# Kernel optimization log

Measured on AMD Instinct MI355X. Metric: run time of the kernel, lower is better.

The kernel has to match this reference:

```python
import jax, jax.numpy as jnp
import numpy as np

N_GAUSS = 1024
IMG = 192
TANFOV = 0.5  # tan(FoV/2), both axes
ZNEAR, ZFAR = 0.01, 100.0

C0 = 0.28209479177387814
C1 = 0.4886025119029199
C2 = (1.0925484305920792, -1.0925484305920792, 0.31539156525252005, -1.0925484305920792, 0.5462742152960396)
C3 = (-0.5900435899266435, 2.890611442640554, -0.4570457994644658, 0.3731763325901154, -0.4570457994644658, 1.445305721320277, -0.5900435899266435)


def _eval_sh3(sh, d):
    # sh: [N,16,3] coeffs, d: [N,3] unit dirs -> clamped rgb [N,3]
    x, y, z = d[:, 0:1], d[:, 1:2], d[:, 2:3]
    xx, yy, zz = x * x, y * y, z * z
    xy, yz, xz = x * y, y * z, x * z
    res = (C0 * sh[:, 0]
           - C1 * y * sh[:, 1] + C1 * z * sh[:, 2] - C1 * x * sh[:, 3]
           + C2[0] * xy * sh[:, 4] + C2[1] * yz * sh[:, 5]
           + C2[2] * (2.0 * zz - xx - yy) * sh[:, 6]
           + C2[3] * xz * sh[:, 7] + C2[4] * (xx - yy) * sh[:, 8]
           + C3[0] * y * (3.0 * xx - yy) * sh[:, 9]
           + C3[1] * xy * z * sh[:, 10]
           + C3[2] * y * (4.0 * zz - xx - yy) * sh[:, 11]
           + C3[3] * z * (2.0 * zz - 3.0 * xx - 3.0 * yy) * sh[:, 12]
           + C3[4] * x * (4.0 * zz - xx - yy) * sh[:, 13]
           + C3[5] * z * (xx - yy) * sh[:, 14]
           + C3[6] * x * (xx - yy - 3.0 * zz) * sh[:, 15])
    return jnp.maximum(res + 0.5, 0.0)


def _quat_to_rot(q):
    r, x, y, z = q[:, 0], q[:, 1], q[:, 2], q[:, 3]
    return jnp.stack([
        1 - 2 * (y * y + z * z), 2 * (x * y - r * z), 2 * (x * z + r * y),
        2 * (x * y + r * z), 1 - 2 * (x * x + z * z), 2 * (y * z - r * x),
        2 * (x * z - r * y), 2 * (y * z + r * x), 1 - 2 * (x * x + y * y),
    ], axis=-1).reshape(-1, 3, 3)


def setup_inputs() -> dict:
    key = jax.random.key(0)
    ks = jax.random.split(key, 6)
    xy = jax.random.uniform(ks[0], (N_GAUSS, 2), minval=-2.0, maxval=2.0)
    z = jax.random.uniform(ks[1], (N_GAUSS, 1), minval=2.0, maxval=10.0)
    means3D = jnp.concatenate([xy, z], axis=1)
    scales = jax.random.uniform(ks[2], (N_GAUSS, 3), minval=0.01, maxval=0.08)
    q = jax.random.normal(ks[3], (N_GAUSS, 4))
    rotations = q / jnp.linalg.norm(q, axis=1, keepdims=True)
    opacities = jax.random.uniform(ks[4], (N_GAUSS, 1), minval=0.1, maxval=0.99)
    shs = jax.random.normal(ks[5], (N_GAUSS, 16, 3)) * 0.3
    viewmatrix = jnp.eye(4, dtype=jnp.float32)
    proj = np.zeros((4, 4), np.float32)
    proj[0, 0] = 1.0 / TANFOV
    proj[1, 1] = 1.0 / TANFOV
    proj[2, 2] = ZFAR / (ZFAR - ZNEAR)
    proj[2, 3] = -ZFAR * ZNEAR / (ZFAR - ZNEAR)
    proj[3, 2] = 1.0
    return dict(means3D=means3D, scales=scales, rotations=rotations,
                opacities=opacities, shs=shs, viewmatrix=viewmatrix,
                projmatrix=jnp.asarray(proj), campos=jnp.zeros(3, jnp.float32),
                bg_color=jnp.zeros(3, jnp.float32),
                image_height=IMG, image_width=IMG)


def reference(means3D, scales, rotations, opacities, shs, viewmatrix,
              projmatrix, campos, bg_color, image_height, image_width):
    H, W = int(image_height), int(image_width)
    fx = W / (2.0 * TANFOV)
    fy = H / (2.0 * TANFOV)
    N = means3D.shape[0]

    # SH -> RGB (convert_SHs_python branch, active_sh_degree = 3)
    dir_pp = means3D - campos[None, :]
    dir_pp = dir_pp / jnp.linalg.norm(dir_pp, axis=1, keepdims=True)
    colors = _eval_sh3(shs, dir_pp)  # [N,3]

    # 3D covariance Sigma = (R S)(R S)^T  (scale_modifier = 1.0)
    R = _quat_to_rot(rotations)
    M = R * scales[:, None, :]
    cov3d = jnp.einsum('nij,nkj->nik', M, M)  # [N,3,3]

    # projection of means
    hom = jnp.concatenate([means3D, jnp.ones((N, 1), means3D.dtype)], axis=1)
    p_view = hom @ viewmatrix.T
    depth = p_view[:, 2]
    p_hom = hom @ projmatrix.T
    p_proj = p_hom[:, :3] / (p_hom[:, 3:4] + 1e-7)
    gx = ((p_proj[:, 0] + 1.0) * W - 1.0) * 0.5  # ndc2Pix
    gy = ((p_proj[:, 1] + 1.0) * H - 1.0) * 0.5
    means2D = jnp.stack([gx, gy], axis=1)

    in_front = depth > 0.2
    tz = jnp.where(in_front, depth, 1.0)
    lim = 1.3 * TANFOV
    tx = jnp.clip(p_view[:, 0] / tz, -lim, lim) * tz
    ty = jnp.clip(p_view[:, 1] / tz, -lim, lim) * tz

    # EWA splatting: J (top 2 rows) composed with view rotation
    zeros = jnp.zeros_like(tz)
    J = jnp.stack([
        jnp.stack([fx / tz, zeros, -fx * tx / (tz * tz)], axis=-1),
        jnp.stack([zeros, fy / tz, -fy * ty / (tz * tz)], axis=-1),
    ], axis=1)  # [N,2,3]
    T = jnp.einsum('nij,jk->nik', J, viewmatrix[:3, :3])
    cov2d = jnp.einsum('nij,njk,nlk->nil', T, cov3d, T)  # [N,2,2]
    a = cov2d[:, 0, 0] + 0.3  # low-pass filter on diagonal
    b = cov2d[:, 0, 1]
    c = cov2d[:, 1, 1] + 0.3

    det = a * c - b * b
    pos_det = det > 0
    inv_det = jnp.where(pos_det, 1.0 / jnp.where(pos_det, det, 1.0), 0.0)
    conA, conB, conC = c * inv_det, -b * inv_det, a * inv_det

    mid = 0.5 * (a + c)
    lam = mid + jnp.sqrt(jnp.maximum(mid * mid - det, 0.1))
    visible = in_front & pos_det
    radii = jnp.where(visible, jnp.ceil(3.0 * jnp.sqrt(lam)), 0.0)
    visibility_filter = radii > 0

    # per-pixel depth-sorted alpha compositing (dense stand-in for tiles)
    yy, xx = jnp.meshgrid(jnp.arange(H, dtype=means3D.dtype),
                          jnp.arange(W, dtype=means3D.dtype), indexing='ij')
    px = xx.reshape(-1)
    py = yy.reshape(-1)
    dx = gx[None, :] - px[:, None]  # [P,N]
    dy = gy[None, :] - py[:, None]
    power = (-0.5 * (conA[None, :] * dx * dx + conC[None, :] * dy * dy)
             - conB[None, :] * dx * dy)
    keep = ((jnp.abs(dx) <= radii[None, :]) & (jnp.abs(dy) <= radii[None, :])
            & visible[None, :] & (power <= 0.0))
    alpha = jnp.minimum(0.99, opacities[:, 0][None, :] * jnp.exp(jnp.minimum(power, 0.0)))
    alpha = jnp.where(keep & (alpha >= 1.0 / 255.0), alpha, 0.0)

    order = jnp.argsort(jnp.where(visible, depth, jnp.inf))
    a_s = alpha[:, order]
    Tcum = jnp.cumprod(1.0 - a_s, axis=1)
    T_before = jnp.concatenate(
        [jnp.ones((a_s.shape[0], 1), a_s.dtype), Tcum[:, :-1]], axis=1)
    wgt = a_s * T_before
    img = wgt @ colors[order] + Tcum[:, -1:] * bg_color[None, :]
    rendered = img.reshape(H, W, 3).transpose(2, 0, 1)  # CHW like torch
    return rendered, radii.astype(jnp.int32), visibility_filter, means2D
```

## Files before the change

kernel.cpp:

```cpp
#include <hip/hip_runtime.h>

#define NG      1024
#define W_IMG   192
#define H_IMG   192
#define HW      (W_IMG * H_IMG)
#define TILES_X 24
#define TILES_Y 24
#define NTILES  (TILES_X * TILES_Y)
#define TPB     256
#define TPBK    4
#define NBLK    (NTILES / TPBK)

__global__ __launch_bounds__(TPB, 1) void render_fused(
    const float* __restrict__ means3D, const float* __restrict__ scales,
    const float* __restrict__ rotations, const float* __restrict__ opacities,
    const float* __restrict__ shs, const float* __restrict__ viewm,
    const float* __restrict__ projm, const float* __restrict__ campos,
    const float* __restrict__ bg, float* __restrict__ outp)
{
    __shared__ float4 sg0[NG];
    __shared__ float4 sg1[NG];
    __shared__ float4 sg2[NG];
    __shared__ unsigned long long skey[TPBK][NG];
    __shared__ unsigned short     ssrt[TPBK][NG];

    const int t = threadIdx.x;

    const float V0 = viewm[0],  V1 = viewm[1],  V2  = viewm[2],  V3  = viewm[3];
    const float V4 = viewm[4],  V5 = viewm[5],  V6  = viewm[6],  V7  = viewm[7];
    const float V8 = viewm[8],  V9 = viewm[9],  V10 = viewm[10], V11 = viewm[11];
    const float P0 = projm[0],  P1 = projm[1],  P2  = projm[2],  P3  = projm[3];
    const float P4 = projm[4],  P5 = projm[5],  P6  = projm[6],  P7  = projm[7];
    const float P12 = projm[12], P13 = projm[13], P14 = projm[14], P15 = projm[15];
    const float CX = campos[0], CY = campos[1], CZ = campos[2];

#pragma unroll
    for (int j = 0; j < NG / TPB; ++j) {
        const int i = t + j * TPB;

        const float mx = means3D[i * 3 + 0];
        const float my = means3D[i * 3 + 1];
        const float mz = means3D[i * 3 + 2];

        float dxc = mx - CX, dyc = my - CY, dzc = mz - CZ;
        float nrm = sqrtf(dxc * dxc + dyc * dyc + dzc * dzc);
        float x = dxc / nrm, y = dyc / nrm, z = dzc / nrm;
        float xx = x * x, yy = y * y, zz = z * z;
        float xy = x * y, yz = y * z, xz = x * z;

        float basis[16];
        basis[0]  = 0.28209479177387814f;
        basis[1]  = -0.4886025119029199f * y;
        basis[2]  =  0.4886025119029199f * z;
        basis[3]  = -0.4886025119029199f * x;
        basis[4]  =  1.0925484305920792f * xy;
        basis[5]  = -1.0925484305920792f * yz;
        basis[6]  =  0.31539156525252005f * (2.f * zz - xx - yy);
        basis[7]  = -1.0925484305920792f * xz;
        basis[8]  =  0.5462742152960396f * (xx - yy);
        basis[9]  = -0.5900435899266435f * y * (3.f * xx - yy);
        basis[10] =  2.890611442640554f  * xy * z;
        basis[11] = -0.4570457994644658f * y * (4.f * zz - xx - yy);
        basis[12] =  0.3731763325901154f * z * (2.f * zz - 3.f * xx - 3.f * yy);
        basis[13] = -0.4570457994644658f * x * (4.f * zz - xx - yy);
        basis[14] =  1.445305721320277f  * z * (xx - yy);
        basis[15] = -0.5900435899266435f * x * (xx - yy - 3.f * zz);

        float sh[48];
        const float4* shv = (const float4*)shs + i * 12;
#pragma unroll
        for (int w = 0; w < 12; ++w) {
            float4 q4 = shv[w];
            sh[4 * w + 0] = q4.x; sh[4 * w + 1] = q4.y;
            sh[4 * w + 2] = q4.z; sh[4 * w + 3] = q4.w;
        }
        float cr = 0.f, cg = 0.f, cb = 0.f;
#pragma unroll
        for (int k = 0; k < 16; ++k) {
            float b = basis[k];
            cr += b * sh[3 * k + 0];
            cg += b * sh[3 * k + 1];
            cb += b * sh[3 * k + 2];
        }
        cr = fmaxf(cr + 0.5f, 0.f);
        cg = fmaxf(cg + 0.5f, 0.f);
        cb = fmaxf(cb + 0.5f, 0.f);

        const float4 q = ((const float4*)rotations)[i];
        float qr = q.x, qx = q.y, qy = q.z, qz = q.w;
        float sx = scales[i * 3 + 0], sy = scales[i * 3 + 1], sz = scales[i * 3 + 2];
        float R00 = 1.f - 2.f * (qy * qy + qz * qz), R01 = 2.f * (qx * qy - qr * qz), R02 = 2.f * (qx * qz + qr * qy);
        float R10 = 2.f * (qx * qy + qr * qz), R11 = 1.f - 2.f * (qx * qx + qz * qz), R12 = 2.f * (qy * qz - qr * qx);
        float R20 = 2.f * (qx * qz - qr * qy), R21 = 2.f * (qy * qz + qr * qx), R22 = 1.f - 2.f * (qx * qx + qy * qy);
        float M00 = R00 * sx, M01 = R01 * sy, M02 = R02 * sz;
        float M10 = R10 * sx, M11 = R11 * sy, M12 = R12 * sz;
        float M20 = R20 * sx, M21 = R21 * sy, M22 = R22 * sz;
        float S00 = M00 * M00 + M01 * M01 + M02 * M02;
        float S01 = M00 * M10 + M01 * M11 + M02 * M12;
        float S02 = M00 * M20 + M01 * M21 + M02 * M22;
        float S11 = M10 * M10 + M11 * M11 + M12 * M12;
        float S12 = M10 * M20 + M11 * M21 + M12 * M22;
        float S22 = M20 * M20 + M21 * M21 + M22 * M22;

        float pv0 = V0 * mx + V1 * my + V2  * mz + V3;
        float pv1 = V4 * mx + V5 * my + V6  * mz + V7;
        float pv2 = V8 * mx + V9 * my + V10 * mz + V11;
        float ph0 = P0  * mx + P1  * my + P2  * mz + P3;
        float ph1 = P4  * mx + P5  * my + P6  * mz + P7;
        float ph3 = P12 * mx + P13 * my + P14 * mz + P15;
        float pp0 = ph0 / (ph3 + 1e-7f);
        float pp1 = ph1 / (ph3 + 1e-7f);
        float gx = ((pp0 + 1.f) * (float)W_IMG - 1.f) * 0.5f;
        float gy = ((pp1 + 1.f) * (float)H_IMG - 1.f) * 0.5f;

        float depth = pv2;
        bool in_front = depth > 0.2f;
        float tz = in_front ? depth : 1.f;
        const float lim = 1.3f * 0.5f;
        float txv = fminf(fmaxf(pv0 / tz, -lim), lim) * tz;
        float tyv = fminf(fmaxf(pv1 / tz, -lim), lim) * tz;
        const float fx = (float)W_IMG / (2.f * 0.5f);
        const float fy = (float)H_IMG / (2.f * 0.5f);
        float J00 = fx / tz, J02 = -fx * txv / (tz * tz);
        float J11 = fy / tz, J12 = -fy * tyv / (tz * tz);

        float T00 = J00 * V0 + J02 * V8;
        float T01 = J00 * V1 + J02 * V9;
        float T02 = J00 * V2 + J02 * V10;
        float T10 = J11 * V4 + J12 * V8;
        float T11 = J11 * V5 + J12 * V9;
        float T12 = J11 * V6 + J12 * V10;

        float u0 = T00 * S00 + T01 * S01 + T02 * S02;
        float u1 = T00 * S01 + T01 * S11 + T02 * S12;
        float u2 = T00 * S02 + T01 * S12 + T02 * S22;
        float w0 = T10 * S00 + T11 * S01 + T12 * S02;
        float w1 = T10 * S01 + T11 * S11 + T12 * S12;
        float w2 = T10 * S02 + T11 * S12 + T12 * S22;
        float c00 = u0 * T00 + u1 * T01 + u2 * T02;
        float c01 = u0 * T10 + u1 * T11 + u2 * T12;
        float c11 = w0 * T10 + w1 * T11 + w2 * T12;

        float a = c00 + 0.3f;
        float b = c01;
        float c = c11 + 0.3f;
        float det = a * c - b * b;
        bool pos_det = det > 0.f;
        float inv_det = pos_det ? 1.f / det : 0.f;
        float conA = c * inv_det, conB = -b * inv_det, conC = a * inv_det;
        float mid = 0.5f * (a + c);
        float lam = mid + sqrtf(fmaxf(mid * mid - det, 0.1f));
        bool visible = in_front && pos_det;
        float radii = visible ? ceilf(3.f * sqrtf(lam)) : 0.f;

        float opa = opacities[i];

        sg0[i] = make_float4(gx, gy, radii, visible ? opa : 0.f);
        sg1[i] = make_float4(conA, conB, conC, depth);
        sg2[i] = make_float4(cr, cg, cb, 0.f);

        if (blockIdx.x == 0) {
            outp[3 * HW + i]              = radii;
            outp[3 * HW + NG + i]         = (radii > 0.f) ? 1.f : 0.f;
            outp[3 * HW + 2 * NG + 2 * i]     = gx;
            outp[3 * HW + 2 * NG + 2 * i + 1] = gy;
        }
    }
    __syncthreads();

    const int wave = t >> 6;
    const int lane = t & 63;
    const int tile = blockIdx.x * TPBK + wave;
    const int tileX = tile % TILES_X;
    const int tileY = tile / TILES_X;
    const float tx0 = (float)(tileX * 8);
    const float ty0 = (float)(tileY * 8);

    int m = 0;
#pragma unroll 4
    for (int it = 0; it < NG / 64; ++it) {
        const int g = it * 64 + lane;
        float4 g0 = sg0[g];
        bool hit = (g0.w > 0.f) &&
                   (g0.x >= tx0 - g0.z) && (g0.x <= tx0 + 7.f + g0.z) &&
                   (g0.y >= ty0 - g0.z) && (g0.y <= ty0 + 7.f + g0.z);
        unsigned long long mask = __ballot(hit);
        if (hit) {
            int pos = m + __popcll(mask & ((1ULL << lane) - 1ULL));
            skey[wave][pos] =
                ((unsigned long long)__float_as_uint(sg1[g].w) << 32) | (unsigned)g;
        }
        m += __popcll(mask);
    }
    __syncthreads();

    for (int s = lane; s < m; s += 64) {
        const unsigned long long ks = skey[wave][s];
        int rank = 0;
        for (int j2 = 0; j2 < m; ++j2)
            rank += (skey[wave][j2] < ks) ? 1 : 0;
        ssrt[wave][rank] = (unsigned short)(ks & 0xFFFFu);
    }
    __syncthreads();

    const int lx = lane & 7, ly = lane >> 3;
    const int pxi = tileX * 8 + lx;
    const int pyi = tileY * 8 + ly;
    const float px = (float)pxi, py = (float)pyi;

    float T = 1.f, accR = 0.f, accG = 0.f, accB = 0.f;
    for (int k = 0; k < m; ++k) {
        const int gi = ssrt[wave][k];
        float4 g0 = sg0[gi];
        float4 g1 = sg1[gi];
        float4 g2 = sg2[gi];
        float dx = g0.x - px, dy = g0.y - py;
        bool cover = (fabsf(dx) <= g0.z) && (fabsf(dy) <= g0.z);
        float power = -0.5f * (g1.x * dx * dx + g1.z * dy * dy) - g1.y * dx * dy;
        float alpha = fminf(0.99f, g0.w * __expf(fminf(power, 0.f)));
        bool keep = cover && (power <= 0.f) && (alpha >= (1.f / 255.f));
        alpha = keep ? alpha : 0.f;
        float w = alpha * T;
        accR += w * g2.x;
        accG += w * g2.y;
        accB += w * g2.z;
        T *= (1.f - alpha);
    }

    const int pix = pyi * W_IMG + pxi;
    outp[pix]          = accR + T * bg[0];
    outp[HW + pix]     = accG + T * bg[1];
    outp[2 * HW + pix] = accB + T * bg[2];
}

extern "C" void kernel_launch(void* const* d_in, const int* in_sizes, int n_in,
                              void* d_out, int out_size, void* d_ws, size_t ws_size,
                              hipStream_t stream)
{
    const float* means3D   = (const float*)d_in[0];
    const float* scales    = (const float*)d_in[1];
    const float* rotations = (const float*)d_in[2];
    const float* opacities = (const float*)d_in[3];
    const float* shs       = (const float*)d_in[4];
    const float* viewm     = (const float*)d_in[5];
    const float* projm     = (const float*)d_in[6];
    const float* campos    = (const float*)d_in[7];
    const float* bg        = (const float*)d_in[8];

    float* outp = (float*)d_out;

    render_fused<<<NBLK, TPB, 0, stream>>>(
        means3D, scales, rotations, opacities, shs, viewm, projm, campos,
        bg, outp);
}
```

Baseline: 88.67 us.

## Evaluate SH colors only for per-tile hit Gaussians after sorting

Moves the spherical-harmonic color evaluation out of the per-block preprocessing of all 1024 Gaussians. Colors are now computed only for the Gaussians that hit each wave's tile, after sorting, and cached in shared memory up to a cap, with a fallback that recomputes them inline beyond the cap. The sort key is also narrowed from 64-bit to a 32-bit depth plus a separate index array, with explicit index tie-breaking. The aim is to cut redundant SH work and the 48-float global load per Gaussian that every block repeated; the cost is divergent per-tile evaluation and possible inline recomputation in the compositing loop for crowded tiles.

```diff
diff --git a/kernel.cpp b/kernel.cpp
--- a/kernel.cpp
+++ b/kernel.cpp
@@ -10,6 +10,59 @@
 #define TPB     256
 #define TPBK    4
 #define NBLK    (NTILES / TPBK)
+#define CMAX    256
+
+__device__ __forceinline__ float3 eval_sh3(
+    const float* __restrict__ shs, const float* __restrict__ means3D,
+    float CX, float CY, float CZ, int i)
+{
+    const float mx = means3D[i * 3 + 0];
+    const float my = means3D[i * 3 + 1];
+    const float mz = means3D[i * 3 + 2];
+    float dxc = mx - CX, dyc = my - CY, dzc = mz - CZ;
+    float nrm = sqrtf(dxc * dxc + dyc * dyc + dzc * dzc);
+    float x = dxc / nrm, y = dyc / nrm, z = dzc / nrm;
+    float xx = x * x, yy = y * y, zz = z * z;
+    float xy = x * y, yz = y * z, xz = x * z;
+
+    float basis[16];
+    basis[0]  = 0.28209479177387814f;
+    basis[1]  = -0.4886025119029199f * y;
+    basis[2]  =  0.4886025119029199f * z;
+    basis[3]  = -0.4886025119029199f * x;
+    basis[4]  =  1.0925484305920792f * xy;
+    basis[5]  = -1.0925484305920792f * yz;
+    basis[6]  =  0.31539156525252005f * (2.f * zz - xx - yy);
+    basis[7]  = -1.0925484305920792f * xz;
+    basis[8]  =  0.5462742152960396f * (xx - yy);
+    basis[9]  = -0.5900435899266435f * y * (3.f * xx - yy);
+    basis[10] =  2.890611442640554f  * xy * z;
+    basis[11] = -0.4570457994644658f * y * (4.f * zz - xx - yy);
+    basis[12] =  0.3731763325901154f * z * (2.f * zz - 3.f * xx - 3.f * yy);
+    basis[13] = -0.4570457994644658f * x * (4.f * zz - xx - yy);
+    basis[14] =  1.445305721320277f  * z * (xx - yy);
+    basis[15] = -0.5900435899266435f * x * (xx - yy - 3.f * zz);
+
+    float sh[48];
+    const float4* shv = (const float4*)shs + i * 12;
+#pragma unroll
+    for (int w = 0; w < 12; ++w) {
+        float4 q4 = shv[w];
+        sh[4 * w + 0] = q4.x; sh[4 * w + 1] = q4.y;
+        sh[4 * w + 2] = q4.z; sh[4 * w + 3] = q4.w;
+    }
+    float cr = 0.f, cg = 0.f, cb = 0.f;
+#pragma unroll
+    for (int k = 0; k < 16; ++k) {
+        float b = basis[k];
+        cr += b * sh[3 * k + 0];
+        cg += b * sh[3 * k + 1];
+        cb += b * sh[3 * k + 2];
+    }
+    return make_float3(fmaxf(cr + 0.5f, 0.f),
+                       fmaxf(cg + 0.5f, 0.f),
+                       fmaxf(cb + 0.5f, 0.f));
+}
 
 __global__ __launch_bounds__(TPB, 1) void render_fused(
     const float* __restrict__ means3D, const float* __restrict__ scales,
@@ -20,9 +73,10 @@
 {
     __shared__ float4 sg0[NG];
     __shared__ float4 sg1[NG];
-    __shared__ float4 sg2[NG];
-    __shared__ unsigned long long skey[TPBK][NG];
-    __shared__ unsigned short     ssrt[TPBK][NG];
+    __shared__ unsigned int   skey[TPBK][NG];
+    __shared__ unsigned short sgi [TPBK][NG];
+    __shared__ unsigned short ssrt[TPBK][NG];
+    __shared__ float4 scol[TPBK][CMAX];
 
     const int t = threadIdx.x;
 
@@ -41,50 +95,6 @@
         const float mx = means3D[i * 3 + 0];
         const float my = means3D[i * 3 + 1];
         const float mz = means3D[i * 3 + 2];
-
-        float dxc = mx - CX, dyc = my - CY, dzc = mz - CZ;
-        float nrm = sqrtf(dxc * dxc + dyc * dyc + dzc * dzc);
-        float x = dxc / nrm, y = dyc / nrm, z = dzc / nrm;
-        float xx = x * x, yy = y * y, zz = z * z;
-        float xy = x * y, yz = y * z, xz = x * z;
-
-        float basis[16];
-        basis[0]  = 0.28209479177387814f;
-        basis[1]  = -0.4886025119029199f * y;
-        basis[2]  =  0.4886025119029199f * z;
-        basis[3]  = -0.4886025119029199f * x;
-        basis[4]  =  1.0925484305920792f * xy;
-        basis[5]  = -1.0925484305920792f * yz;
-        basis[6]  =  0.31539156525252005f * (2.f * zz - xx - yy);
-        basis[7]  = -1.0925484305920792f * xz;
-        basis[8]  =  0.5462742152960396f * (xx - yy);
-        basis[9]  = -0.5900435899266435f * y * (3.f * xx - yy);
-        basis[10] =  2.890611442640554f  * xy * z;
-        basis[11] = -0.4570457994644658f * y * (4.f * zz - xx - yy);
-        basis[12] =  0.3731763325901154f * z * (2.f * zz - 3.f * xx - 3.f * yy);
-        basis[13] = -0.4570457994644658f * x * (4.f * zz - xx - yy);
-        basis[14] =  1.445305721320277f  * z * (xx - yy);
-        basis[15] = -0.5900435899266435f * x * (xx - yy - 3.f * zz);
-
-        float sh[48];
-        const float4* shv = (const float4*)shs + i * 12;
-#pragma unroll
-        for (int w = 0; w < 12; ++w) {
-            float4 q4 = shv[w];
-            sh[4 * w + 0] = q4.x; sh[4 * w + 1] = q4.y;
-            sh[4 * w + 2] = q4.z; sh[4 * w + 3] = q4.w;
-        }
-        float cr = 0.f, cg = 0.f, cb = 0.f;
-#pragma unroll
-        for (int k = 0; k < 16; ++k) {
-            float b = basis[k];
-            cr += b * sh[3 * k + 0];
-            cg += b * sh[3 * k + 1];
-            cb += b * sh[3 * k + 2];
-        }
-        cr = fmaxf(cr + 0.5f, 0.f);
-        cg = fmaxf(cg + 0.5f, 0.f);
-        cb = fmaxf(cb + 0.5f, 0.f);
 
         const float4 q = ((const float4*)rotations)[i];
         float qr = q.x, qx = q.y, qy = q.z, qz = q.w;
@@ -157,7 +167,6 @@
 
         sg0[i] = make_float4(gx, gy, radii, visible ? opa : 0.f);
         sg1[i] = make_float4(conA, conB, conC, depth);
-        sg2[i] = make_float4(cr, cg, cb, 0.f);
 
         if (blockIdx.x == 0) {
             outp[3 * HW + i]              = radii;
@@ -187,19 +196,29 @@
         unsigned long long mask = __ballot(hit);
         if (hit) {
             int pos = m + __popcll(mask & ((1ULL << lane) - 1ULL));
-            skey[wave][pos] =
-                ((unsigned long long)__float_as_uint(sg1[g].w) << 32) | (unsigned)g;
+            skey[wave][pos] = __float_as_uint(sg1[g].w);
+            sgi [wave][pos] = (unsigned short)g;
         }
         m += __popcll(mask);
     }
     __syncthreads();
 
     for (int s = lane; s < m; s += 64) {
-        const unsigned long long ks = skey[wave][s];
+        const unsigned int ks = skey[wave][s];
         int rank = 0;
-        for (int j2 = 0; j2 < m; ++j2)
-            rank += (skey[wave][j2] < ks) ? 1 : 0;
-        ssrt[wave][rank] = (unsigned short)(ks & 0xFFFFu);
+        for (int j2 = 0; j2 < m; ++j2) {
+            unsigned int kj = skey[wave][j2];
+            rank += (kj < ks || (kj == ks && j2 < s)) ? 1 : 0;
+        }
+        ssrt[wave][rank] = sgi[wave][s];
+    }
+    __syncthreads();
+
+    const int mc = (m < CMAX) ? m : CMAX;
+    for (int s = lane; s < mc; s += 64) {
+        const int gi = ssrt[wave][s];
+        float3 col = eval_sh3(shs, means3D, CX, CY, CZ, gi);
+        scol[wave][s] = make_float4(col.x, col.y, col.z, 0.f);
     }
     __syncthreads();
 
@@ -213,7 +232,13 @@
         const int gi = ssrt[wave][k];
         float4 g0 = sg0[gi];
         float4 g1 = sg1[gi];
-        float4 g2 = sg2[gi];
+        float3 col;
+        if (k < CMAX) {
+            float4 c4 = scol[wave][k];
+            col = make_float3(c4.x, c4.y, c4.z);
+        } else {
+            col = eval_sh3(shs, means3D, CX, CY, CZ, gi);
+        }
         float dx = g0.x - px, dy = g0.y - py;
         bool cover = (fabsf(dx) <= g0.z) && (fabsf(dy) <= g0.z);
         float power = -0.5f * (g1.x * dx * dx + g1.z * dy * dy) - g1.y * dx * dy;
@@ -221,9 +246,9 @@
         bool keep = cover && (power <= 0.f) && (alpha >= (1.f / 255.f));
         alpha = keep ? alpha : 0.f;
         float w = alpha * T;
-        accR += w * g2.x;
-        accG += w * g2.y;
-        accB += w * g2.z;
+        accR += w * col.x;
+        accG += w * col.y;
+        accB += w * col.z;
         T *= (1.f - alpha);
     }
 
```

After: 88.73 us. No clear change (+0.1%).

## Split fused renderer into global preprocess kernel and per-tile raster kernel

Applied to the files above, without the earlier changes.

The single fused kernel made all 144 blocks redundantly preprocess all 1024 Gaussians into shared memory. This splits the work into a preprocess kernel that runs once per Gaussian and writes to a workspace, followed by a raster kernel with one 64-thread block per tile. The raster kernel compacts the hit Gaussians' parameters into shared memory (up to 256) with 32-bit depth keys and stable rank ties, falling back to global reads for overflow. The cost is an extra kernel launch and a global round trip for the preprocessed data.

```diff
diff --git a/kernel.cpp b/kernel.cpp
--- a/kernel.cpp
+++ b/kernel.cpp
@@ -7,170 +7,161 @@
 #define TILES_X 24
 #define TILES_Y 24
 #define NTILES  (TILES_X * TILES_Y)
-#define TPB     256
-#define TPBK    4
-#define NBLK    (NTILES / TPBK)
-
-__global__ __launch_bounds__(TPB, 1) void render_fused(
+#define SMAX    256
+
+
+__global__ __launch_bounds__(64) void preprocess_kernel(
     const float* __restrict__ means3D, const float* __restrict__ scales,
     const float* __restrict__ rotations, const float* __restrict__ opacities,
     const float* __restrict__ shs, const float* __restrict__ viewm,
     const float* __restrict__ projm, const float* __restrict__ campos,
-    const float* __restrict__ bg, float* __restrict__ outp)
+    float4* __restrict__ pg0, float4* __restrict__ pg1,
+    float4* __restrict__ pcol, float* __restrict__ outp)
 {
-    __shared__ float4 sg0[NG];
-    __shared__ float4 sg1[NG];
-    __shared__ float4 sg2[NG];
-    __shared__ unsigned long long skey[TPBK][NG];
-    __shared__ unsigned short     ssrt[TPBK][NG];
-
-    const int t = threadIdx.x;
-
-    const float V0 = viewm[0],  V1 = viewm[1],  V2  = viewm[2],  V3  = viewm[3];
-    const float V4 = viewm[4],  V5 = viewm[5],  V6  = viewm[6],  V7  = viewm[7];
-    const float V8 = viewm[8],  V9 = viewm[9],  V10 = viewm[10], V11 = viewm[11];
-    const float P0 = projm[0],  P1 = projm[1],  P2  = projm[2],  P3  = projm[3];
-    const float P4 = projm[4],  P5 = projm[5],  P6  = projm[6],  P7  = projm[7];
-    const float P12 = projm[12], P13 = projm[13], P14 = projm[14], P15 = projm[15];
-    const float CX = campos[0], CY = campos[1], CZ = campos[2];
-
+    const int i = blockIdx.x * 64 + threadIdx.x;
+    if (i >= NG) return;
+
+    const float mx = means3D[i * 3 + 0];
+    const float my = means3D[i * 3 + 1];
+    const float mz = means3D[i * 3 + 2];
+
+    float dxc = mx - campos[0], dyc = my - campos[1], dzc = mz - campos[2];
+    float nrm = sqrtf(dxc * dxc + dyc * dyc + dzc * dzc);
+    float x = dxc / nrm, y = dyc / nrm, z = dzc / nrm;
+    float xx = x * x, yy = y * y, zz = z * z;
+    float xy = x * y, yz = y * z, xz = x * z;
+
+    float basis[16];
+    basis[0]  = 0.28209479177387814f;
+    basis[1]  = -0.4886025119029199f * y;
+    basis[2]  =  0.4886025119029199f * z;
+    basis[3]  = -0.4886025119029199f * x;
+    basis[4]  =  1.0925484305920792f * xy;
+    basis[5]  = -1.0925484305920792f * yz;
+    basis[6]  =  0.31539156525252005f * (2.f * zz - xx - yy);
+    basis[7]  = -1.0925484305920792f * xz;
+    basis[8]  =  0.5462742152960396f * (xx - yy);
+    basis[9]  = -0.5900435899266435f * y * (3.f * xx - yy);
+    basis[10] =  2.890611442640554f  * xy * z;
+    basis[11] = -0.4570457994644658f * y * (4.f * zz - xx - yy);
+    basis[12] =  0.3731763325901154f * z * (2.f * zz - 3.f * xx - 3.f * yy);
+    basis[13] = -0.4570457994644658f * x * (4.f * zz - xx - yy);
+    basis[14] =  1.445305721320277f  * z * (xx - yy);
+    basis[15] = -0.5900435899266435f * x * (xx - yy - 3.f * zz);
+
+    float sh[48];
+    const float4* shv = (const float4*)shs + i * 12;
 #pragma unroll
-    for (int j = 0; j < NG / TPB; ++j) {
-        const int i = t + j * TPB;
-
-        const float mx = means3D[i * 3 + 0];
-        const float my = means3D[i * 3 + 1];
-        const float mz = means3D[i * 3 + 2];
-
-        float dxc = mx - CX, dyc = my - CY, dzc = mz - CZ;
-        float nrm = sqrtf(dxc * dxc + dyc * dyc + dzc * dzc);
-        float x = dxc / nrm, y = dyc / nrm, z = dzc / nrm;
-        float xx = x * x, yy = y * y, zz = z * z;
-        float xy = x * y, yz = y * z, xz = x * z;
-
-        float basis[16];
-        basis[0]  = 0.28209479177387814f;
-        basis[1]  = -0.4886025119029199f * y;
-        basis[2]  =  0.4886025119029199f * z;
-        basis[3]  = -0.4886025119029199f * x;
-        basis[4]  =  1.0925484305920792f * xy;
-        basis[5]  = -1.0925484305920792f * yz;
-        basis[6]  =  0.31539156525252005f * (2.f * zz - xx - yy);
-        basis[7]  = -1.0925484305920792f * xz;
-        basis[8]  =  0.5462742152960396f * (xx - yy);
-        basis[9]  = -0.5900435899266435f * y * (3.f * xx - yy);
-        basis[10] =  2.890611442640554f  * xy * z;
-        basis[11] = -0.4570457994644658f * y * (4.f * zz - xx - yy);
-        basis[12] =  0.3731763325901154f * z * (2.f * zz - 3.f * xx - 3.f * yy);
-        basis[13] = -0.4570457994644658f * x * (4.f * zz - xx - yy);
-        basis[14] =  1.445305721320277f  * z * (xx - yy);
-        basis[15] = -0.5900435899266435f * x * (xx - yy - 3.f * zz);
-
-        float sh[48];
-        const float4* shv = (const float4*)shs + i * 12;
+    for (int w = 0; w < 12; ++w) {
+        float4 q4 = shv[w];
+        sh[4 * w + 0] = q4.x; sh[4 * w + 1] = q4.y;
+        sh[4 * w + 2] = q4.z; sh[4 * w + 3] = q4.w;
+    }
+    float cr = 0.f, cg = 0.f, cb = 0.f;
 #pragma unroll
-        for (int w = 0; w < 12; ++w) {
-            float4 q4 = shv[w];
-            sh[4 * w + 0] = q4.x; sh[4 * w + 1] = q4.y;
-            sh[4 * w + 2] = q4.z; sh[4 * w + 3] = q4.w;
-        }
-        float cr = 0.f, cg = 0.f, cb = 0.f;
-#pragma unroll
-        for (int k = 0; k < 16; ++k) {
-            float b = basis[k];
-            cr += b * sh[3 * k + 0];
-            cg += b * sh[3 * k + 1];
-            cb += b * sh[3 * k + 2];
-        }
-        cr = fmaxf(cr + 0.5f, 0.f);
-        cg = fmaxf(cg + 0.5f, 0.f);
-        cb = fmaxf(cb + 0.5f, 0.f);
-
-        const float4 q = ((const float4*)rotations)[i];
-        float qr = q.x, qx = q.y, qy = q.z, qz = q.w;
-        float sx = scales[i * 3 + 0], sy = scales[i * 3 + 1], sz = scales[i * 3 + 2];
-        float R00 = 1.f - 2.f * (qy * qy + qz * qz), R01 = 2.f * (qx * qy - qr * qz), R02 = 2.f * (qx * qz + qr * qy);
-        float R10 = 2.f * (qx * qy + qr * qz), R11 = 1.f - 2.f * (qx * qx + qz * qz), R12 = 2.f * (qy * qz - qr * qx);
-        float R20 = 2.f * (qx * qz - qr * qy), R21 = 2.f * (qy * qz + qr * qx), R22 = 1.f - 2.f * (qx * qx + qy * qy);
-        float M00 = R00 * sx, M01 = R01 * sy, M02 = R02 * sz;
-        float M10 = R10 * sx, M11 = R11 * sy, M12 = R12 * sz;
-        float M20 = R20 * sx, M21 = R21 * sy, M22 = R22 * sz;
-        float S00 = M00 * M00 + M01 * M01 + M02 * M02;
-        float S01 = M00 * M10 + M01 * M11 + M02 * M12;
-        float S02 = M00 * M20 + M01 * M21 + M02 * M22;
-        float S11 = M10 * M10 + M11 * M11 + M12 * M12;
-        float S12 = M10 * M20 + M11 * M21 + M12 * M22;
-        float S22 = M20 * M20 + M21 * M21 + M22 * M22;
-
-        float pv0 = V0 * mx + V1 * my + V2  * mz + V3;
-        float pv1 = V4 * mx + V5 * my + V6  * mz + V7;
-        float pv2 = V8 * mx + V9 * my + V10 * mz + V11;
-        float ph0 = P0  * mx + P1  * my + P2  * mz + P3;
-        float ph1 = P4  * mx + P5  * my + P6  * mz + P7;
-        float ph3 = P12 * mx + P13 * my + P14 * mz + P15;
-        float pp0 = ph0 / (ph3 + 1e-7f);
-        float pp1 = ph1 / (ph3 + 1e-7f);
-        float gx = ((pp0 + 1.f) * (float)W_IMG - 1.f) * 0.5f;
-        float gy = ((pp1 + 1.f) * (float)H_IMG - 1.f) * 0.5f;
-
-        float depth = pv2;
-        bool in_front = depth > 0.2f;
-        float tz = in_front ? depth : 1.f;
-        const float lim = 1.3f * 0.5f;
-        float txv = fminf(fmaxf(pv0 / tz, -lim), lim) * tz;
-        float tyv = fminf(fmaxf(pv1 / tz, -lim), lim) * tz;
-        const float fx = (float)W_IMG / (2.f * 0.5f);
-        const float fy = (float)H_IMG / (2.f * 0.5f);
-        float J00 = fx / tz, J02 = -fx * txv / (tz * tz);
-        float J11 = fy / tz, J12 = -fy * tyv / (tz * tz);
-
-        float T00 = J00 * V0 + J02 * V8;
-        float T01 = J00 * V1 + J02 * V9;
-        float T02 = J00 * V2 + J02 * V10;
-        float T10 = J11 * V4 + J12 * V8;
-        float T11 = J11 * V5 + J12 * V9;
-        float T12 = J11 * V6 + J12 * V10;
-
-        float u0 = T00 * S00 + T01 * S01 + T02 * S02;
-        float u1 = T00 * S01 + T01 * S11 + T02 * S12;
-        float u2 = T00 * S02 + T01 * S12 + T02 * S22;
-        float w0 = T10 * S00 + T11 * S01 + T12 * S02;
-        float w1 = T10 * S01 + T11 * S11 + T12 * S12;
-        float w2 = T10 * S02 + T11 * S12 + T12 * S22;
-        float c00 = u0 * T00 + u1 * T01 + u2 * T02;
-        float c01 = u0 * T10 + u1 * T11 + u2 * T12;
-        float c11 = w0 * T10 + w1 * T11 + w2 * T12;
-
-        float a = c00 + 0.3f;
-        float b = c01;
-        float c = c11 + 0.3f;
-        float det = a * c - b * b;
-        bool pos_det = det > 0.f;
-        float inv_det = pos_det ? 1.f / det : 0.f;
-        float conA = c * inv_det, conB = -b * inv_det, conC = a * inv_det;
-        float mid = 0.5f * (a + c);
-        float lam = mid + sqrtf(fmaxf(mid * mid - det, 0.1f));
-        bool visible = in_front && pos_det;
-        float radii = visible ? ceilf(3.f * sqrtf(lam)) : 0.f;
-
-        float opa = opacities[i];
-
-        sg0[i] = make_float4(gx, gy, radii, visible ? opa : 0.f);
-        sg1[i] = make_float4(conA, conB, conC, depth);
-        sg2[i] = make_float4(cr, cg, cb, 0.f);
-
-        if (blockIdx.x == 0) {
-            outp[3 * HW + i]              = radii;
-            outp[3 * HW + NG + i]         = (radii > 0.f) ? 1.f : 0.f;
-            outp[3 * HW + 2 * NG + 2 * i]     = gx;
-            outp[3 * HW + 2 * NG + 2 * i + 1] = gy;
-        }
-    }
-    __syncthreads();
-
-    const int wave = t >> 6;
-    const int lane = t & 63;
-    const int tile = blockIdx.x * TPBK + wave;
+    for (int k = 0; k < 16; ++k) {
+        float b = basis[k];
+        cr += b * sh[3 * k + 0];
+        cg += b * sh[3 * k + 1];
+        cb += b * sh[3 * k + 2];
+    }
+    cr = fmaxf(cr + 0.5f, 0.f);
+    cg = fmaxf(cg + 0.5f, 0.f);
+    cb = fmaxf(cb + 0.5f, 0.f);
+
+    const float4 q = ((const float4*)rotations)[i];
+    float qr = q.x, qx = q.y, qy = q.z, qz = q.w;
+    float sx = scales[i * 3 + 0], sy = scales[i * 3 + 1], sz = scales[i * 3 + 2];
+    float R00 = 1.f - 2.f * (qy * qy + qz * qz), R01 = 2.f * (qx * qy - qr * qz), R02 = 2.f * (qx * qz + qr * qy);
+    float R10 = 2.f * (qx * qy + qr * qz), R11 = 1.f - 2.f * (qx * qx + qz * qz), R12 = 2.f * (qy * qz - qr * qx);
+    float R20 = 2.f * (qx * qz - qr * qy), R21 = 2.f * (qy * qz + qr * qx), R22 = 1.f - 2.f * (qx * qx + qy * qy);
+    float M00 = R00 * sx, M01 = R01 * sy, M02 = R02 * sz;
+    float M10 = R10 * sx, M11 = R11 * sy, M12 = R12 * sz;
+    float M20 = R20 * sx, M21 = R21 * sy, M22 = R22 * sz;
+    float S00 = M00 * M00 + M01 * M01 + M02 * M02;
+    float S01 = M00 * M10 + M01 * M11 + M02 * M12;
+    float S02 = M00 * M20 + M01 * M21 + M02 * M22;
+    float S11 = M10 * M10 + M11 * M11 + M12 * M12;
+    float S12 = M10 * M20 + M11 * M21 + M12 * M22;
+    float S22 = M20 * M20 + M21 * M21 + M22 * M22;
+
+    float pv0 = viewm[0] * mx + viewm[1] * my + viewm[2]  * mz + viewm[3];
+    float pv1 = viewm[4] * mx + viewm[5] * my + viewm[6]  * mz + viewm[7];
+    float pv2 = viewm[8] * mx + viewm[9] * my + viewm[10] * mz + viewm[11];
+    float ph0 = projm[0]  * mx + projm[1]  * my + projm[2]  * mz + projm[3];
+    float ph1 = projm[4]  * mx + projm[5]  * my + projm[6]  * mz + projm[7];
+    float ph3 = projm[12] * mx + projm[13] * my + projm[14] * mz + projm[15];
+    float pp0 = ph0 / (ph3 + 1e-7f);
+    float pp1 = ph1 / (ph3 + 1e-7f);
+    float gx = ((pp0 + 1.f) * (float)W_IMG - 1.f) * 0.5f;
+    float gy = ((pp1 + 1.f) * (float)H_IMG - 1.f) * 0.5f;
+
+    float depth = pv2;
+    bool in_front = depth > 0.2f;
+    float tz = in_front ? depth : 1.f;
+    const float lim = 1.3f * 0.5f;
+    float txv = fminf(fmaxf(pv0 / tz, -lim), lim) * tz;
+    float tyv = fminf(fmaxf(pv1 / tz, -lim), lim) * tz;
+    const float fx = (float)W_IMG / (2.f * 0.5f);
+    const float fy = (float)H_IMG / (2.f * 0.5f);
+    float J00 = fx / tz, J02 = -fx * txv / (tz * tz);
+    float J11 = fy / tz, J12 = -fy * tyv / (tz * tz);
+
+    float T00 = J00 * viewm[0] + J02 * viewm[8];
+    float T01 = J00 * viewm[1] + J02 * viewm[9];
+    float T02 = J00 * viewm[2] + J02 * viewm[10];
+    float T10 = J11 * viewm[4] + J12 * viewm[8];
+    float T11 = J11 * viewm[5] + J12 * viewm[9];
+    float T12 = J11 * viewm[6] + J12 * viewm[10];
+
+    float u0 = T00 * S00 + T01 * S01 + T02 * S02;
+    float u1 = T00 * S01 + T01 * S11 + T02 * S12;
+    float u2 = T00 * S02 + T01 * S12 + T02 * S22;
+    float v0 = T10 * S00 + T11 * S01 + T12 * S02;
+    float v1 = T10 * S01 + T11 * S11 + T12 * S12;
+    float v2 = T10 * S02 + T11 * S12 + T12 * S22;
+    float c00 = u0 * T00 + u1 * T01 + u2 * T02;
+    float c01 = u0 * T10 + u1 * T11 + u2 * T12;
+    float c11 = v0 * T10 + v1 * T11 + v2 * T12;
+
+    float a = c00 + 0.3f;
+    float b = c01;
+    float c = c11 + 0.3f;
+    float det = a * c - b * b;
+    bool pos_det = det > 0.f;
+    float inv_det = pos_det ? 1.f / det : 0.f;
+    float conA = c * inv_det, conB = -b * inv_det, conC = a * inv_det;
+    float mid = 0.5f * (a + c);
+    float lam = mid + sqrtf(fmaxf(mid * mid - det, 0.1f));
+    bool visible = in_front && pos_det;
+    float radii = visible ? ceilf(3.f * sqrtf(lam)) : 0.f;
+
+    float opa = opacities[i];
+
+    outp[3 * HW + i]              = radii;
+    outp[3 * HW + NG + i]         = (radii > 0.f) ? 1.f : 0.f;
+    outp[3 * HW + 2 * NG + 2 * i]     = gx;
+    outp[3 * HW + 2 * NG + 2 * i + 1] = gy;
+
+    pg0[i]  = make_float4(gx, gy, radii, visible ? opa : 0.f);
+    pg1[i]  = make_float4(conA, conB, conC, depth);
+    pcol[i] = make_float4(cr, cg, cb, 0.f);
+}
+
+__global__ __launch_bounds__(64) void raster_kernel(
+    const float4* __restrict__ pg0, const float4* __restrict__ pg1,
+    const float4* __restrict__ pcol, const float* __restrict__ bg,
+    float* __restrict__ outp)
+{
+    __shared__ unsigned int   skey[NG];
+    __shared__ unsigned short sgi [NG];
+    __shared__ unsigned short ssrt[NG];
+    __shared__ float4 sr0[SMAX];
+    __shared__ float4 sr1[SMAX];
+    __shared__ float4 sc [SMAX];
+
+    const int lane  = threadIdx.x;
+    const int tile  = blockIdx.x;
     const int tileX = tile % TILES_X;
     const int tileY = tile / TILES_X;
     const float tx0 = (float)(tileX * 8);
@@ -180,26 +171,34 @@
 #pragma unroll 4
     for (int it = 0; it < NG / 64; ++it) {
         const int g = it * 64 + lane;
-        float4 g0 = sg0[g];
+        float4 g0 = pg0[g];
         bool hit = (g0.w > 0.f) &&
                    (g0.x >= tx0 - g0.z) && (g0.x <= tx0 + 7.f + g0.z) &&
                    (g0.y >= ty0 - g0.z) && (g0.y <= ty0 + 7.f + g0.z);
         unsigned long long mask = __ballot(hit);
         if (hit) {
             int pos = m + __popcll(mask & ((1ULL << lane) - 1ULL));
-            skey[wave][pos] =
-                ((unsigned long long)__float_as_uint(sg1[g].w) << 32) | (unsigned)g;
+            float4 g1 = pg1[g];
+            skey[pos] = __float_as_uint(g1.w);
+            sgi [pos] = (unsigned short)g;
+            if (pos < SMAX) {
+                sr0[pos] = g0;
+                sr1[pos] = g1;
+                sc [pos] = pcol[g];
+            }
         }
         m += __popcll(mask);
     }
     __syncthreads();
 
     for (int s = lane; s < m; s += 64) {
-        const unsigned long long ks = skey[wave][s];
+        const unsigned int ks = skey[s];
         int rank = 0;
-        for (int j2 = 0; j2 < m; ++j2)
-            rank += (skey[wave][j2] < ks) ? 1 : 0;
-        ssrt[wave][rank] = (unsigned short)(ks & 0xFFFFu);
+        for (int j = 0; j < m; ++j) {
+            unsigned int kj = skey[j];
+            rank += (kj < ks || (kj == ks && j < s)) ? 1 : 0;
+        }
+        ssrt[rank] = (unsigned short)s;
     }
     __syncthreads();
 
@@ -210,10 +209,14 @@
 
     float T = 1.f, accR = 0.f, accG = 0.f, accB = 0.f;
     for (int k = 0; k < m; ++k) {
-        const int gi = ssrt[wave][k];
-        float4 g0 = sg0[gi];
-        float4 g1 = sg1[gi];
-        float4 g2 = sg2[gi];
+        const int p = ssrt[k];
+        float4 g0, g1, cl;
+        if (p < SMAX) {
+            g0 = sr0[p]; g1 = sr1[p]; cl = sc[p];
+        } else {
+            const int gi = sgi[p];
+            g0 = pg0[gi]; g1 = pg1[gi]; cl = pcol[gi];
+        }
         float dx = g0.x - px, dy = g0.y - py;
         bool cover = (fabsf(dx) <= g0.z) && (fabsf(dy) <= g0.z);
         float power = -0.5f * (g1.x * dx * dx + g1.z * dy * dy) - g1.y * dx * dy;
@@ -221,9 +224,9 @@
         bool keep = cover && (power <= 0.f) && (alpha >= (1.f / 255.f));
         alpha = keep ? alpha : 0.f;
         float w = alpha * T;
-        accR += w * g2.x;
-        accG += w * g2.y;
-        accB += w * g2.z;
+        accR += w * cl.x;
+        accG += w * cl.y;
+        accB += w * cl.z;
         T *= (1.f - alpha);
     }
 
@@ -247,9 +250,14 @@
     const float* campos    = (const float*)d_in[7];
     const float* bg        = (const float*)d_in[8];
 
-    float* outp = (float*)d_out;
-
-    render_fused<<<NBLK, TPB, 0, stream>>>(
+    float*  outp = (float*)d_out;
+    float4* pg0  = (float4*)d_ws;
+    float4* pg1  = pg0 + NG;
+    float4* pcol = pg0 + 2 * NG;
+
+    preprocess_kernel<<<NG / 64, 64, 0, stream>>>(
         means3D, scales, rotations, opacities, shs, viewm, projm, campos,
-        bg, outp);
+        pg0, pg1, pcol, outp);
+
+    raster_kernel<<<NTILES, 64, 0, stream>>>(pg0, pg1, pcol, bg, outp);
 }
```

New measurement: 91.74 us. +3.5%, slower.
